# Performance work log

Measured on AMD Instinct MI355X. Metric: run time of the kernel, lower is better.

## Reference

```python
import jax, jax.numpy as jnp
import numpy as np

TAU = 1.0
PAD_IDX = 0
EOS_IDX = 3
NEG = -10000000.0

B, T, H, E, V, BN = 256, 256, 1024, 512, 32000, 512


def setup_inputs() -> dict:
    key = jax.random.key(0)
    ks = jax.random.split(key, 30)
    s = lambda *sh: 0.02
    inp = {}
    inp['input_ids'] = jax.random.randint(ks[0], (B,), 0, V)
    inp['prediction'] = jax.random.normal(ks[1], (B, V), jnp.float32)
    inp['context'] = jax.random.normal(ks[2], (B, T, 2 * H), jnp.float32)
    inp['h0'] = jax.random.normal(ks[3], (2, B, H), jnp.float32)
    inp['mask'] = jax.random.randint(ks[4], (B, 8), 0, V)
    # parameters
    inp['embedding'] = jax.random.normal(ks[5], (V, E), jnp.float32) * 0.02
    inp['ge1_w'] = jax.random.normal(ks[6], (E, E), jnp.float32) * 0.02
    inp['ge1_b'] = jnp.zeros((E,), jnp.float32)
    inp['ge2_w'] = jax.random.normal(ks[7], (E, E), jnp.float32) * 0.02
    inp['ge2_b'] = jnp.zeros((E,), jnp.float32)
    inp['att_we'] = jax.random.normal(ks[8], (2 * H, H), jnp.float32) * 0.02
    inp['att_wd'] = jax.random.normal(ks[9], (H, H), jnp.float32) * 0.02
    inp['att_v'] = jax.random.normal(ks[10], (H,), jnp.float32) * 0.02
    in0 = 2 * H + E
    inp['wih0'] = jax.random.normal(ks[11], (3 * H, in0), jnp.float32) * 0.02
    inp['whh0'] = jax.random.normal(ks[12], (3 * H, H), jnp.float32) * 0.02
    inp['bih0'] = jnp.zeros((3 * H,), jnp.float32)
    inp['bhh0'] = jnp.zeros((3 * H,), jnp.float32)
    inp['wih1'] = jax.random.normal(ks[13], (3 * H, H), jnp.float32) * 0.02
    inp['whh1'] = jax.random.normal(ks[14], (3 * H, H), jnp.float32) * 0.02
    inp['bih1'] = jnp.zeros((3 * H,), jnp.float32)
    inp['bhh1'] = jnp.zeros((3 * H,), jnp.float32)
    inp['bn0_w'] = jax.random.normal(ks[15], (3 * H + E, BN), jnp.float32) * 0.02
    inp['bn0_b'] = jnp.zeros((BN,), jnp.float32)
    inp['bn1_w'] = jax.random.normal(ks[16], (BN, V), jnp.float32) * 0.02
    inp['bn1_b'] = jnp.zeros((V,), jnp.float32)
    return inp


def _gru_cell(x, h, wih, whh, bih, bhh):
    gi = x @ wih.T + bih  # [B, 3H]
    gh = h @ whh.T + bhh
    gi_r, gi_z, gi_n = jnp.split(gi, 3, axis=1)
    gh_r, gh_z, gh_n = jnp.split(gh, 3, axis=1)
    r = jax.nn.sigmoid(gi_r + gh_r)
    z = jax.nn.sigmoid(gi_z + gh_z)
    n = jnp.tanh(gi_n + r * gh_n)
    return (1.0 - z) * n + z * h


def _forward(input_ids, prediction, context, h0, mask, embedding,
             ge1_w, ge1_b, ge2_w, ge2_b, att_we, att_wd, att_v,
             wih0, whh0, bih0, bhh0, wih1, whh1, bih1, bhh1,
             bn0_w, bn0_b, bn1_w, bn1_b):
    embs = embedding[input_ids]  # [B, E]
    # global embedding gate
    probs = jax.nn.softmax(prediction / TAU, axis=1)  # [B, V]
    emb_avg = probs @ embedding  # [B, E]
    Hg = jax.nn.sigmoid(embs @ ge1_w + ge1_b + emb_avg @ ge2_w + ge2_b)
    embs = Hg * embs + (1.0 - Hg) * emb_avg
    # bahdanau attention with query = top-layer hidden
    q = h0[-1]  # [B, H]
    scores = jnp.tanh(context @ att_we + (q @ att_wd)[:, None, :]) @ att_v  # [B, T]
    attn = jax.nn.softmax(scores, axis=1)
    c_t = jnp.einsum('bt,btd->bd', attn, context)  # [B, 2H]
    rnn_in = jnp.concatenate([embs, c_t], axis=1)  # [B, E+2H]
    h1_0 = _gru_cell(rnn_in, h0[0], wih0, whh0, bih0, bhh0)
    h1_1 = _gru_cell(h1_0, h0[1], wih1, whh1, bih1, bhh1)
    output = h1_1
    h1 = jnp.stack([h1_0, h1_1])
    b0 = jnp.tanh(jnp.concatenate([output, c_t, embs], axis=1) @ bn0_w + bn0_b)
    pred = b0 @ bn1_w + bn1_b  # [B, V]
    # masked scatter: forbid already-generated tokens, but keep PAD/EOS columns
    pad_col = pred[:, PAD_IDX]
    eos_col = pred[:, EOS_IDX]
    rows = jnp.arange(pred.shape[0])
    pred = pred.at[rows[:, None], mask].set(NEG)
    pred = pred.at[:, PAD_IDX].set(pad_col)
    pred = pred.at[:, EOS_IDX].set(eos_col)
    return pred, h1, attn


def reference(input_ids, prediction, context, h0, mask, embedding,
              ge1_w, ge1_b, ge2_w, ge2_b, att_we, att_wd, att_v,
              wih0, whh0, bih0, bhh0, wih1, whh1, bih1, bhh1,
              bn0_w, bn0_b, bn1_w, bn1_b):
    return _forward(input_ids, prediction, context, h0, mask, embedding,
                    ge1_w, ge1_b, ge2_w, ge2_b, att_we, att_wd, att_v,
                    wih0, whh0, bih0, bhh0, wih1, whh1, bih1, bhh1,
                    bn0_w, bn0_b, bn1_w, bn1_b)
```

## Files before the change

kernel.cpp:

```cpp
#include <hip/hip_runtime.h>
#include <hip/hip_bf16.h>


typedef unsigned short u16;
typedef unsigned int u32;
typedef float f32x4 __attribute__((ext_vector_type(4)));
typedef u32 u32x4 __attribute__((ext_vector_type(4)));
typedef __bf16 bf16x8 __attribute__((ext_vector_type(8)));
typedef short s16x8 __attribute__((ext_vector_type(8)));

__device__ __forceinline__ u16 f2bf(float x) {
  u32 u = __float_as_uint(x);
  u += 0x7fffu + ((u >> 16) & 1u);
  return (u16)(u >> 16);
}
__device__ __forceinline__ u32 pack2(float a, float b) {
  return (u32)f2bf(a) | ((u32)f2bf(b) << 16);
}
__device__ __forceinline__ u32 cvt2(float a, float b) {
  union { __bf16 h[2]; u32 w; } u;
  u.h[0] = (__bf16)a; u.h[1] = (__bf16)b;
  return u.w;
}
__device__ __forceinline__ float bf2f(u16 v) {
  return __uint_as_float((u32)v << 16);
}
__device__ __forceinline__ f32x4 mfma_bf16(s16x8 a, s16x8 b, f32x4 c) {
  union { s16x8 s; bf16x8 b; } ua, ub;
  ua.s = a; ub.s = b;
  return __builtin_amdgcn_mfma_f32_16x16x32_bf16(ua.b, ub.b, c, 0, 0, 0);
}
__device__ __forceinline__ void gll16(const void* g, void* l) {
  __builtin_amdgcn_global_load_lds((__attribute__((address_space(1))) void*)g,
                                   (__attribute__((address_space(3))) void*)l,
                                   16, 0, 0);
}
__device__ __forceinline__ float sigf(float x) { return 1.0f / (1.0f + __expf(-x)); }

__global__ __launch_bounds__(256) void k_cvt8(const float* __restrict__ s,
                                              u16* __restrict__ d)
{
  size_t i = ((size_t)blockIdx.x * 256 + threadIdx.x) * 8;
  const size_t stride = (size_t)gridDim.x * 2048;
  for (; i < 134217728ull; i += stride) {
    float4 a = *(const float4*)(s + i);
    float4 b = *(const float4*)(s + i + 4);
    u32x4 w = {cvt2(a.x, a.y), cvt2(a.z, a.w), cvt2(b.x, b.y), cvt2(b.z, b.w)};
    *(u32x4*)(d + i) = w;
  }
}

__global__ __launch_bounds__(256, 2) void k_scores_bf(
    const u16* __restrict__ A, const u16* __restrict__ weT,
    const float* __restrict__ qd, const float* __restrict__ att_v,
    float* __restrict__ scores)
{
  __shared__ u16 As[3][4096];
  __shared__ u16 Bs[3][8192];

  const int tid = threadIdx.x;
  const int lane = tid & 63, wid = tid >> 6;
  const int l15 = lane & 15, lg = lane >> 4;
  const int wm = wid >> 1, wn = wid & 1;

  const int f = blockIdx.x;
  const int xcd = f & 7, slot = f >> 3;
  const int ntile = slot & 3;
  const int mtile = (slot >> 2) * 8 + xcd;
  const int n0 = ntile * 256;
  const int m0 = mtile * 128;
  const int b = mtile >> 1;

  const int sslot = ((lane & 3) ^ ((lane >> 3) & 3)) * 8;
  size_t asrc[2];
#pragma unroll
  for (int i = 0; i < 2; ++i)
    asrc[i] = (size_t)(m0 + wid * 32 + i * 16 + (lane >> 2)) * 2048 + sslot;
  size_t bsrc[4];
#pragma unroll
  for (int i = 0; i < 4; ++i)
    bsrc[i] = (size_t)(n0 + wid * 64 + i * 16 + (lane >> 2)) * 2048 + sslot;

  const int rslot = (lg ^ ((l15 >> 1) & 3)) * 8;
  int aoff[4], boff[8];
#pragma unroll
  for (int mf = 0; mf < 4; ++mf) aoff[mf] = (wm * 64 + mf * 16 + l15) * 32 + rslot;
#pragma unroll
  for (int nf = 0; nf < 8; ++nf) boff[nf] = (wn * 128 + nf * 16 + l15) * 32 + rslot;

  f32x4 acc[4][8];
#pragma unroll
  for (int mf = 0; mf < 4; ++mf)
#pragma unroll
    for (int nf = 0; nf < 8; ++nf) acc[mf][nf] = (f32x4){0.f, 0.f, 0.f, 0.f};

  u16* As0 = &As[0][0];
  u16* Bs0 = &Bs[0][0];

#pragma unroll
  for (int t = 0; t < 2; ++t) {
#pragma unroll
    for (int i = 0; i < 2; ++i)
      gll16(A + asrc[i] + (size_t)t * 32, As0 + t * 4096 + wid * 1024 + i * 512);
#pragma unroll
    for (int i = 0; i < 4; ++i)
      gll16(weT + bsrc[i] + (size_t)t * 32, Bs0 + t * 8192 + wid * 2048 + i * 512);
  }

  int cur = 0, stg = 2;
  for (int kt = 0; kt < 64; ++kt) {
    if (kt < 63) asm volatile("s_waitcnt vmcnt(6)" ::: "memory");
    else         asm volatile("s_waitcnt vmcnt(0)" ::: "memory");
    __builtin_amdgcn_s_barrier();
    __builtin_amdgcn_sched_barrier(0);
    if (kt + 2 < 64) {
#pragma unroll
      for (int i = 0; i < 2; ++i)
        gll16(A + asrc[i] + (size_t)(kt + 2) * 32,
              As0 + stg * 4096 + wid * 1024 + i * 512);
#pragma unroll
      for (int i = 0; i < 4; ++i)
        gll16(weT + bsrc[i] + (size_t)(kt + 2) * 32,
              Bs0 + stg * 8192 + wid * 2048 + i * 512);
    }
    s16x8 af[4], bf[8];
#pragma unroll
    for (int mf = 0; mf < 4; ++mf)
      af[mf] = *(const s16x8*)(As0 + cur * 4096 + aoff[mf]);
#pragma unroll
    for (int nf = 0; nf < 8; ++nf)
      bf[nf] = *(const s16x8*)(Bs0 + cur * 8192 + boff[nf]);
    __builtin_amdgcn_s_setprio(1);
#pragma unroll
    for (int nf = 0; nf < 8; ++nf)
#pragma unroll
      for (int mf = 0; mf < 4; ++mf)
        acc[mf][nf] = mfma_bf16(af[mf], bf[nf], acc[mf][nf]);
    __builtin_amdgcn_s_setprio(0);
    cur = (cur == 2) ? 0 : cur + 1;
    stg = (stg == 2) ? 0 : stg + 1;
  }

  float rp[4][4] = {{0.f, 0.f, 0.f, 0.f}, {0.f, 0.f, 0.f, 0.f},
                    {0.f, 0.f, 0.f, 0.f}, {0.f, 0.f, 0.f, 0.f}};
#pragma unroll
  for (int nf = 0; nf < 8; ++nf) {
    int col = n0 + wn * 128 + nf * 16 + l15;
    float qv = qd[(size_t)b * 1024 + col];
    float vv = att_v[col];
#pragma unroll
    for (int mf = 0; mf < 4; ++mf)
#pragma unroll
      for (int e = 0; e < 4; ++e)
        rp[mf][e] += tanhf(acc[mf][nf][e] + qv) * vv;
  }
#pragma unroll
  for (int d = 1; d < 16; d <<= 1)
#pragma unroll
    for (int mf = 0; mf < 4; ++mf)
#pragma unroll
      for (int e = 0; e < 4; ++e)
        rp[mf][e] += __shfl_xor(rp[mf][e], d);
  if (l15 == 0) {
#pragma unroll
    for (int mf = 0; mf < 4; ++mf)
#pragma unroll
      for (int e = 0; e < 4; ++e)
        atomicAdd(&scores[(size_t)m0 + wm * 64 + mf * 16 + lg * 4 + e], rp[mf][e]);
  }
}

__global__ __launch_bounds__(256, 3) void k_scores(
    const float* __restrict__ ctx, const u16* __restrict__ weT,
    const float* __restrict__ qd, const float* __restrict__ att_v,
    float* __restrict__ scores)
{
  __shared__ u16 As[2][4096];
  __shared__ u16 Bs[2][4096];

  const int tid = threadIdx.x;
  const int lane = tid & 63, wid = tid >> 6;
  const int l15 = lane & 15, lg = lane >> 4;
  const int wm = wid >> 1, wn = wid & 1;
  const int n0 = blockIdx.x * 128;
  const int m0 = blockIdx.y * 128;
  const int b = blockIdx.y >> 1;

  const int r0 = tid >> 3, c4 = tid & 7;
  const float* actx = ctx + (size_t)(m0 + r0) * 2048 + c4 * 4;
  const int awoff = r0 * 32 + c4 * 4;

  size_t bsrc[2];
#pragma unroll
  for (int i = 0; i < 2; ++i)
    bsrc[i] = (size_t)(n0 + (wid * 2 + i) * 16 + (lane >> 2)) * 2048 + (size_t)(lane & 3) * 8;

  int aoff[4], boff[4];
#pragma unroll
  for (int mf = 0; mf < 4; ++mf) aoff[mf] = (wm * 64 + mf * 16 + l15) * 32 + lg * 8;
#pragma unroll
  for (int nf = 0; nf < 4; ++nf) boff[nf] = (wn * 64 + nf * 16 + l15) * 32 + lg * 8;

  f32x4 acc[4][4];
#pragma unroll
  for (int mf = 0; mf < 4; ++mf)
#pragma unroll
    for (int nf = 0; nf < 4; ++nf) acc[mf][nf] = (f32x4){0.f, 0.f, 0.f, 0.f};

  {
#pragma unroll
    for (int i = 0; i < 2; ++i)
      gll16(weT + bsrc[i], &Bs[0][(wid * 2 + i) * 512]);
#pragma unroll
    for (int j = 0; j < 4; ++j) {
      float4 av = *(const float4*)(actx + (size_t)(j * 32) * 2048);
      u32* w = (u32*)&As[0][awoff + j * 1024];
      w[0] = cvt2(av.x, av.y); w[1] = cvt2(av.z, av.w);
    }
  }
  __syncthreads();

  for (int kt = 0; kt < 64; ++kt) {
    const int cur = kt & 1, nxt = cur ^ 1;
    const bool pf = (kt < 63);
    float4 av[4];
    if (pf) {
#pragma unroll
      for (int i = 0; i < 2; ++i)
        gll16(weT + bsrc[i] + (size_t)(kt + 1) * 32, &Bs[nxt][(wid * 2 + i) * 512]);
#pragma unroll
      for (int j = 0; j < 4; ++j)
        av[j] = *(const float4*)(actx + (size_t)(j * 32) * 2048 + (kt + 1) * 32);
    }
    s16x8 af[4], bf[4];
#pragma unroll
    for (int mf = 0; mf < 4; ++mf) af[mf] = *(const s16x8*)(&As[cur][0] + aoff[mf]);
#pragma unroll
    for (int nf = 0; nf < 4; ++nf) bf[nf] = *(const s16x8*)(&Bs[cur][0] + boff[nf]);
#pragma unroll
    for (int nf = 0; nf < 4; ++nf)
#pragma unroll
      for (int mf = 0; mf < 4; ++mf)
        acc[mf][nf] = mfma_bf16(af[mf], bf[nf], acc[mf][nf]);
    if (pf) {
#pragma unroll
      for (int j = 0; j < 4; ++j) {
        u32* w = (u32*)&As[nxt][awoff + j * 1024];
        w[0] = cvt2(av[j].x, av[j].y); w[1] = cvt2(av[j].z, av[j].w);
      }
    }
    __syncthreads();
  }

  float rp[4][4] = {{0.f, 0.f, 0.f, 0.f}, {0.f, 0.f, 0.f, 0.f},
                    {0.f, 0.f, 0.f, 0.f}, {0.f, 0.f, 0.f, 0.f}};
#pragma unroll
  for (int nf = 0; nf < 4; ++nf) {
    int col = n0 + wn * 64 + nf * 16 + l15;
    float qv = qd[(size_t)b * 1024 + col];
    float vv = att_v[col];
#pragma unroll
    for (int mf = 0; mf < 4; ++mf)
#pragma unroll
      for (int e = 0; e < 4; ++e)
        rp[mf][e] += tanhf(acc[mf][nf][e] + qv) * vv;
  }
#pragma unroll
  for (int d = 1; d < 16; d <<= 1)
#pragma unroll
    for (int mf = 0; mf < 4; ++mf)
#pragma unroll
      for (int e = 0; e < 4; ++e)
        rp[mf][e] += __shfl_xor(rp[mf][e], d);
  if (l15 == 0) {
#pragma unroll
    for (int mf = 0; mf < 4; ++mf)
#pragma unroll
      for (int e = 0; e < 4; ++e)
        atomicAdd(&scores[(size_t)m0 + wm * 64 + mf * 16 + lg * 4 + e], rp[mf][e]);
  }
}

template <int MODE>
__global__ __launch_bounds__(256, 2) void k_gemm(
    const u16* __restrict__ A, const float* __restrict__ W,
    float* __restrict__ C, const float* __restrict__ bias,
    int N, int K, int ksteps_per, int tot_ksteps, int atomic_mode)
{
  __shared__ u16 As[2][8192];
  __shared__ u16 Bs[2][2048];
  const int tid = threadIdx.x, lane = tid & 63, wid = tid >> 6;
  const int l15 = lane & 15, lg = lane >> 4;
  const int m0 = blockIdx.x * 256;
  const int n0 = blockIdx.y * 64;
  const int kc0 = blockIdx.z * ksteps_per;
  int kcn = tot_ksteps - kc0;
  if (kcn > ksteps_per) kcn = ksteps_per;

  size_t asrc[4];
#pragma unroll
  for (int j = 0; j < 4; ++j)
    asrc[j] = (size_t)(m0 + wid * 64 + j * 16 + (lane >> 2)) * K + (size_t)(lane & 3) * 8;
  int aoff[4], boff[4];
#pragma unroll
  for (int mf = 0; mf < 4; ++mf) aoff[mf] = (wid * 64 + mf * 16 + l15) * 32 + lg * 8;
#pragma unroll
  for (int nf = 0; nf < 4; ++nf) boff[nf] = (nf * 16 + l15) * 32 + lg * 8;

  const int b_row = tid >> 2, b_c8 = tid & 3;
  const int b_kk = tid >> 3, b_c4 = tid & 7;

  f32x4 acc[4][4];
#pragma unroll
  for (int mf = 0; mf < 4; ++mf)
#pragma unroll
    for (int nf = 0; nf < 4; ++nf) acc[mf][nf] = (f32x4){0.f, 0.f, 0.f, 0.f};

  {
#pragma unroll
    for (int j = 0; j < 4; ++j)
      gll16(A + asrc[j] + (size_t)kc0 * 32, &As[0][wid * 2048 + j * 512]);
    if (MODE == 0) {
      const float* p = W + (size_t)(n0 + b_row) * K + (size_t)kc0 * 32 + b_c8 * 8;
      float4 v0 = *(const float4*)p, v1 = *(const float4*)(p + 4);
      u32* w = (u32*)&Bs[0][b_row * 32 + b_c8 * 8];
      w[0] = pack2(v0.x, v0.y); w[1] = pack2(v0.z, v0.w);
      w[2] = pack2(v1.x, v1.y); w[3] = pack2(v1.z, v1.w);
    } else {
      const float* p = W + (size_t)(kc0 * 32 + b_kk) * N + n0 + b_c4 * 4;
      float4 v0 = *(const float4*)p;
      float4 v1 = *(const float4*)(p + 32);
      int r0 = b_c4 * 4, r1 = 32 + b_c4 * 4;
      Bs[0][(r0 + 0) * 32 + b_kk] = f2bf(v0.x);
      Bs[0][(r0 + 1) * 32 + b_kk] = f2bf(v0.y);
      Bs[0][(r0 + 2) * 32 + b_kk] = f2bf(v0.z);
      Bs[0][(r0 + 3) * 32 + b_kk] = f2bf(v0.w);
      Bs[0][(r1 + 0) * 32 + b_kk] = f2bf(v1.x);
      Bs[0][(r1 + 1) * 32 + b_kk] = f2bf(v1.y);
      Bs[0][(r1 + 2) * 32 + b_kk] = f2bf(v1.z);
      Bs[0][(r1 + 3) * 32 + b_kk] = f2bf(v1.w);
    }
  }
  __syncthreads();

  for (int s = 0; s < kcn; ++s) {
    const int cur = s & 1, nxt = cur ^ 1;
    const bool pf = (s + 1 < kcn);
    const int ktn = kc0 + s + 1;
    float4 v0, v1;
    if (pf) {
#pragma unroll
      for (int j = 0; j < 4; ++j)
        gll16(A + asrc[j] + (size_t)ktn * 32, &As[nxt][wid * 2048 + j * 512]);
      if (MODE == 0) {
        const float* p = W + (size_t)(n0 + b_row) * K + (size_t)ktn * 32 + b_c8 * 8;
        v0 = *(const float4*)p; v1 = *(const float4*)(p + 4);
      } else {
        const float* p = W + (size_t)(ktn * 32 + b_kk) * N + n0 + b_c4 * 4;
        v0 = *(const float4*)p;
        v1 = *(const float4*)(p + 32);
      }
    }
    s16x8 af[4], bf[4];
#pragma unroll
    for (int mf = 0; mf < 4; ++mf) af[mf] = *(const s16x8*)(&As[cur][0] + aoff[mf]);
#pragma unroll
    for (int nf = 0; nf < 4; ++nf) bf[nf] = *(const s16x8*)(&Bs[cur][0] + boff[nf]);
#pragma unroll
    for (int nf = 0; nf < 4; ++nf)
#pragma unroll
      for (int mf = 0; mf < 4; ++mf)
        acc[mf][nf] = mfma_bf16(af[mf], bf[nf], acc[mf][nf]);
    if (pf) {
      if (MODE == 0) {
        u32* w = (u32*)&Bs[nxt][b_row * 32 + b_c8 * 8];
        w[0] = pack2(v0.x, v0.y); w[1] = pack2(v0.z, v0.w);
        w[2] = pack2(v1.x, v1.y); w[3] = pack2(v1.z, v1.w);
      } else {
        int r0 = b_c4 * 4, r1 = 32 + b_c4 * 4;
        Bs[nxt][(r0 + 0) * 32 + b_kk] = f2bf(v0.x);
        Bs[nxt][(r0 + 1) * 32 + b_kk] = f2bf(v0.y);
        Bs[nxt][(r0 + 2) * 32 + b_kk] = f2bf(v0.z);
        Bs[nxt][(r0 + 3) * 32 + b_kk] = f2bf(v0.w);
        Bs[nxt][(r1 + 0) * 32 + b_kk] = f2bf(v1.x);
        Bs[nxt][(r1 + 1) * 32 + b_kk] = f2bf(v1.y);
        Bs[nxt][(r1 + 2) * 32 + b_kk] = f2bf(v1.z);
        Bs[nxt][(r1 + 3) * 32 + b_kk] = f2bf(v1.w);
      }
    }
    __syncthreads();
  }

  const size_t Ns = (size_t)N;
#pragma unroll
  for (int mf = 0; mf < 4; ++mf)
#pragma unroll
    for (int nf = 0; nf < 4; ++nf) {
      int col = n0 + nf * 16 + l15;
#pragma unroll
      for (int e = 0; e < 4; ++e) {
        int row = m0 + wid * 64 + mf * 16 + lg * 4 + e;
        float v = acc[mf][nf][e];
        if (atomic_mode) atomicAdd(&C[row * Ns + col], v);
        else C[row * Ns + col] = v + (bias ? bias[col] : 0.0f);
      }
    }
}

__global__ __launch_bounds__(256) void k_prep(
    const float* __restrict__ we, u16* __restrict__ weT,
    const float* __restrict__ h0, u16* __restrict__ h0_bf,
    const int* __restrict__ ids, const float* __restrict__ emb,
    float* __restrict__ e0, u16* __restrict__ e0b)
{
  __shared__ float t[32][33];
  const int bid = blockIdx.x, tid = threadIdx.x;
  if (bid < 2048) {
    const int n0 = (bid & 31) * 32, k0 = (bid >> 5) * 32;
#pragma unroll
    for (int p = 0; p < 4; ++p) {
      int e = tid + p * 256, r = e >> 5, c = e & 31;
      t[r][c] = we[(size_t)(k0 + r) * 1024 + n0 + c];
    }
    __syncthreads();
#pragma unroll
    for (int p = 0; p < 4; ++p) {
      int e = tid + p * 256, n = e >> 5, k = e & 31;
      weT[(size_t)(n0 + n) * 2048 + k0 + k] = f2bf(t[k][n]);
    }
  } else if (bid < 4096) {
    int i = (bid - 2048) * 256 + tid;
    h0_bf[i] = f2bf(h0[i]);
  } else {
    int b = bid - 4096;
    int id = ids[b];
    for (int i = tid; i < 512; i += 256) {
      float v = emb[(size_t)id * 512 + i];
      e0[(size_t)b * 512 + i] = v;
      e0b[(size_t)b * 512 + i] = f2bf(v);
    }
  }
}

__global__ void k_cast(const float* __restrict__ s, u16* __restrict__ d, int n)
{
  int i = blockIdx.x * 256 + threadIdx.x;
  if (i < n) d[i] = f2bf(s[i]);
}

__global__ __launch_bounds__(1024) void k_softmax_pred(const float* __restrict__ pred,
                                                       u16* __restrict__ probs)
{
  __shared__ u16 xrow[32000];
  __shared__ float smM[16], smS[16];
  const int row = blockIdx.x, tid = threadIdx.x;
  const float* x = pred + (size_t)row * 32000;
  float m = -3.0e38f, s = 0.f;
  for (int i = tid; i < 32000; i += 1024) {
    u16 bv = f2bf(x[i]);
    xrow[i] = bv;
    float vr = bf2f(bv);
    if (vr > m) { s = s * __expf(m - vr) + 1.0f; m = vr; }
    else s += __expf(vr - m);
  }
#pragma unroll
  for (int d = 1; d < 64; d <<= 1) {
    float mo = __shfl_xor(m, d), so = __shfl_xor(s, d);
    float M = fmaxf(m, mo);
    s = s * __expf(m - M) + so * __expf(mo - M);
    m = M;
  }
  if ((tid & 63) == 0) { smM[tid >> 6] = m; smS[tid >> 6] = s; }
  __syncthreads();
  float M = -3.0e38f;
#pragma unroll
  for (int w = 0; w < 16; ++w) M = fmaxf(M, smM[w]);
  float S = 0.f;
#pragma unroll
  for (int w = 0; w < 16; ++w) S += smS[w] * __expf(smM[w] - M);
  float inv = 1.0f / S;
  for (int i = tid; i < 32000; i += 1024)
    probs[(size_t)row * 32000 + i] = f2bf(__expf(bf2f(xrow[i]) - M) * inv);
}

__global__ __launch_bounds__(256) void k_softmax_sc(const float* __restrict__ sc,
                                                    float* __restrict__ attn)
{
  __shared__ float sm[4];
  const int row = blockIdx.x, tid = threadIdx.x;
  float x = sc[(size_t)row * 256 + tid];
  float mx = x;
#pragma unroll
  for (int d = 1; d < 64; d <<= 1) mx = fmaxf(mx, __shfl_xor(mx, d));
  if ((tid & 63) == 0) sm[tid >> 6] = mx;
  __syncthreads();
  mx = fmaxf(fmaxf(sm[0], sm[1]), fmaxf(sm[2], sm[3]));
  float e = __expf(x - mx);
  float s = e;
#pragma unroll
  for (int d = 1; d < 64; d <<= 1) s += __shfl_xor(s, d);
  __syncthreads();
  if ((tid & 63) == 0) sm[tid >> 6] = s;
  __syncthreads();
  s = sm[0] + sm[1] + sm[2] + sm[3];
  attn[(size_t)row * 256 + tid] = e / s;
}

__global__ __launch_bounds__(256) void k_attn_ct(
    const float* __restrict__ sc, const u16* __restrict__ ctxb,
    float* __restrict__ attn, float* __restrict__ c_t)
{
  __shared__ float sm[4];
  __shared__ float att[256];
  const int b = blockIdx.y, tid = threadIdx.x;
  float x = sc[(size_t)b * 256 + tid];
  float mx = x;
#pragma unroll
  for (int d = 1; d < 64; d <<= 1) mx = fmaxf(mx, __shfl_xor(mx, d));
  if ((tid & 63) == 0) sm[tid >> 6] = mx;
  __syncthreads();
  mx = fmaxf(fmaxf(sm[0], sm[1]), fmaxf(sm[2], sm[3]));
  float e = __expf(x - mx);
  float s = e;
#pragma unroll
  for (int d = 1; d < 64; d <<= 1) s += __shfl_xor(s, d);
  __syncthreads();
  if ((tid & 63) == 0) sm[tid >> 6] = s;
  __syncthreads();
  s = sm[0] + sm[1] + sm[2] + sm[3];
  float a = e / s;
  att[tid] = a;
  if (blockIdx.x == 0) attn[(size_t)b * 256 + tid] = a;
  __syncthreads();

  const int d0 = blockIdx.x * 512 + tid * 2;
  const u16* cp = ctxb + (size_t)b * 524288 + d0;
  float a0 = 0.f, a1 = 0.f;
#pragma unroll 8
  for (int t = 0; t < 256; ++t) {
    float av = att[t];
    ushort2 v = *(const ushort2*)(cp + (size_t)t * 2048);
    a0 += av * bf2f(v.x); a1 += av * bf2f(v.y);
  }
  float2* o = (float2*)(c_t + (size_t)b * 2048 + d0);
  *o = (float2){a0, a1};
}

__global__ __launch_bounds__(256) void k_ct(const float* __restrict__ ctx,
                                            const float* __restrict__ attn,
                                            float* __restrict__ c_t)
{
  const int b = blockIdx.y;
  const int d0 = blockIdx.x * 512 + threadIdx.x * 2;
  const float2* cp = (const float2*)(ctx + (size_t)b * 524288 + d0);
  const float* ar = attn + (size_t)b * 256;
  float ax = 0.f, ay = 0.f;
#pragma unroll 4
  for (int t = 0; t < 256; ++t) {
    float a = ar[t];
    float2 v = cp[(size_t)t * 1024];
    ax += a * v.x; ay += a * v.y;
  }
  c_t[(size_t)b * 2048 + d0] = ax;
  c_t[(size_t)b * 2048 + d0 + 1] = ay;
}

__global__ void k_gate_cat(const float* __restrict__ gepre, const float* __restrict__ b1,
                           const float* __restrict__ b2, const float* __restrict__ e0,
                           const float* __restrict__ ea, float* __restrict__ embs,
                           const float* __restrict__ ct, u16* __restrict__ out)
{
  int i = blockIdx.x * 256 + threadIdx.x;
  int m = i / 2560, c = i - m * 2560;
  float v;
  if (c < 512) {
    int idx = m * 512 + c;
    float hg = sigf(gepre[idx] + b1[c] + b2[c]);
    v = hg * e0[idx] + (1.0f - hg) * ea[idx];
    embs[idx] = v;
  } else {
    v = ct[(size_t)m * 2048 + (c - 512)];
  }
  out[i] = f2bf(v);
}

__global__ void k_gru(const float* __restrict__ gi, const float* __restrict__ gh,
                      const float* __restrict__ bih, const float* __restrict__ bhh,
                      const float* __restrict__ hprev, float* __restrict__ hout,
                      u16* __restrict__ hout_bf)
{
  int i = blockIdx.x * 256 + threadIdx.x;
  int m = i >> 10, h = i & 1023;
  const float* gim = gi + (size_t)m * 3072;
  const float* ghm = gh + (size_t)m * 3072;
  float r = sigf(gim[h] + bih[h] + ghm[h] + bhh[h]);
  float z = sigf(gim[1024 + h] + bih[1024 + h] + ghm[1024 + h] + bhh[1024 + h]);
  float n = tanhf(gim[2048 + h] + bih[2048 + h] + r * (ghm[2048 + h] + bhh[2048 + h]));
  float hv = (1.0f - z) * n + z * hprev[i];
  hout[i] = hv;
  if (hout_bf) hout_bf[i] = f2bf(hv);
}

__global__ void k_cat_bn0(const float* __restrict__ h11, const float* __restrict__ ct,
                          const float* __restrict__ embs, u16* __restrict__ out)
{
  int i = blockIdx.x * 256 + threadIdx.x;
  int m = i / 3584, c = i - m * 3584;
  float v;
  if (c < 1024) v = h11[(size_t)m * 1024 + c];
  else if (c < 3072) v = ct[(size_t)m * 2048 + (c - 1024)];
  else v = embs[(size_t)m * 512 + (c - 3072)];
  out[i] = f2bf(v);
}

__global__ void k_bn0(const float* __restrict__ pre, const float* __restrict__ bias,
                      u16* __restrict__ b0b)
{
  int i = blockIdx.x * 256 + threadIdx.x;
  int nn = i & 511;
  b0b[i] = f2bf(tanhf(pre[i] + bias[nn]));
}

__global__ void k_mask(const int* __restrict__ mask, float* __restrict__ pred)
{
  int t = blockIdx.x * 256 + threadIdx.x;
  if (t >= 2048) return;
  int b = t >> 3;
  int col = mask[t];
  if (col != 0 && col != 3) pred[(size_t)b * 32000 + col] = -10000000.0f;
}

extern "C" void kernel_launch(void* const* d_in, const int* in_sizes, int n_in,
                              void* d_out, int out_size, void* d_ws, size_t ws_size,
                              hipStream_t stream)
{
  const int*   input_ids = (const int*)d_in[0];
  const float* prediction= (const float*)d_in[1];
  const float* context   = (const float*)d_in[2];
  const float* h0        = (const float*)d_in[3];
  const int*   maskp     = (const int*)d_in[4];
  const float* embedding = (const float*)d_in[5];
  const float* ge1_w = (const float*)d_in[6];
  const float* ge1_b = (const float*)d_in[7];
  const float* ge2_w = (const float*)d_in[8];
  const float* ge2_b = (const float*)d_in[9];
  const float* att_we = (const float*)d_in[10];
  const float* att_wd = (const float*)d_in[11];
  const float* att_v  = (const float*)d_in[12];
  const float* wih0 = (const float*)d_in[13];
  const float* whh0 = (const float*)d_in[14];
  const float* bih0 = (const float*)d_in[15];
  const float* bhh0 = (const float*)d_in[16];
  const float* wih1 = (const float*)d_in[17];
  const float* whh1 = (const float*)d_in[18];
  const float* bih1 = (const float*)d_in[19];
  const float* bhh1 = (const float*)d_in[20];
  const float* bn0_w = (const float*)d_in[21];
  const float* bn0_b = (const float*)d_in[22];
  const float* bn1_w = (const float*)d_in[23];
  const float* bn1_b = (const float*)d_in[24];

  float* out = (float*)d_out;
  float* out_pred = out;
  float* out_h1_0 = out + 8192000;
  float* out_h1_1 = out + 8454144;
  float* out_attn = out + 8716288;

  char* ws = (char*)d_ws;
  float* qd      = (float*)(ws + 0);
  float* emb_avg = (float*)(ws + 1048576);
  float* gepre   = (float*)(ws + 1572864);
  float* gi0     = (float*)(ws + 2097152);
  float* gh0     = (float*)(ws + 5242880);
  float* gi1     = (float*)(ws + 8388608);
  float* gh1     = (float*)(ws + 11534336);
  float* bn0pre  = (float*)(ws + 14680064);
  float* scores  = (float*)(ws + 15204352);
  const size_t MS_BYTES = 15466496;
  float* c_t     = (float*)(ws + 15466496);
  float* embs0   = (float*)(ws + 17563648);
  float* embs    = (float*)(ws + 18087936);
  u16* weT       = (u16*)(ws + 18612224);
  u16* h0_bf     = (u16*)(ws + 22806528);
  u16* embs0_bf  = (u16*)(ws + 23855104);
  u16* probs_bf  = (u16*)(ws + 24117248);
  u16* embavg_bf = (u16*)(ws + 40501248);
  u16* rnnin_bf  = (u16*)(ws + 40763392);
  u16* h1_0_bf   = (u16*)(ws + 42074112);
  u16* bn0in_bf  = (u16*)(ws + 42598400);
  u16* b0_bf     = (u16*)(ws + 44433408);
  u16* ctx_bf    = (u16*)(ws + 44695552);
  const bool big = ws_size >= 44695552ull + 268435456ull;

  (void)in_sizes; (void)n_in; (void)out_size;

  hipMemsetAsync(ws, 0, MS_BYTES, stream);

  if (big) k_cvt8<<<8192, 256, 0, stream>>>(context, ctx_bf);
  k_prep<<<4352, 256, 0, stream>>>(att_we, weT, h0, h0_bf, input_ids, embedding,
                                   embs0, embs0_bf);
  k_softmax_pred<<<256, 1024, 0, stream>>>(prediction, probs_bf);

  k_gemm<1><<<dim3(1, 16, 8), 256, 0, stream>>>(h0_bf + 262144, att_wd, qd, nullptr,
                                                1024, 1024, 4, 32, 1);
  if (big)
    k_scores_bf<<<2048, 256, 0, stream>>>(ctx_bf, weT, qd, att_v, scores);
  else
    k_scores<<<dim3(8, 512), 256, 0, stream>>>(context, weT, qd, att_v, scores);

  k_gemm<1><<<dim3(1, 8, 50), 256, 0, stream>>>(probs_bf, embedding, emb_avg, nullptr,
                                                512, 32000, 20, 1000, 1);
  k_cast<<<512, 256, 0, stream>>>(emb_avg, embavg_bf, 131072);
  k_gemm<1><<<dim3(1, 8, 4), 256, 0, stream>>>(embs0_bf, ge1_w, gepre, nullptr,
                                               512, 512, 4, 16, 1);
  k_gemm<1><<<dim3(1, 8, 4), 256, 0, stream>>>(embavg_bf, ge2_w, gepre, nullptr,
                                               512, 512, 4, 16, 1);

  if (big) {
    k_attn_ct<<<dim3(4, 256), 256, 0, stream>>>(scores, ctx_bf, out_attn, c_t);
  } else {
    k_softmax_sc<<<256, 256, 0, stream>>>(scores, out_attn);
    k_ct<<<dim3(4, 256), 256, 0, stream>>>(context, out_attn, c_t);
  }

  k_gate_cat<<<2560, 256, 0, stream>>>(gepre, ge1_b, ge2_b, embs0, emb_avg,
                                       embs, c_t, rnnin_bf);

  k_gemm<0><<<dim3(1, 48, 5), 256, 0, stream>>>(rnnin_bf, wih0, gi0, nullptr,
                                                3072, 2560, 16, 80, 1);
  k_gemm<0><<<dim3(1, 48, 4), 256, 0, stream>>>(h0_bf, whh0, gh0, nullptr,
                                                3072, 1024, 8, 32, 1);
  k_gru<<<1024, 256, 0, stream>>>(gi0, gh0, bih0, bhh0, h0, out_h1_0, h1_0_bf);
  k_gemm<0><<<dim3(1, 48, 4), 256, 0, stream>>>(h1_0_bf, wih1, gi1, nullptr,
                                                3072, 1024, 8, 32, 1);
  k_gemm<0><<<dim3(1, 48, 4), 256, 0, stream>>>(h0_bf + 262144, whh1, gh1, nullptr,
                                                3072, 1024, 8, 32, 1);
  k_gru<<<1024, 256, 0, stream>>>(gi1, gh1, bih1, bhh1, h0 + 262144, out_h1_1, nullptr);

  k_cat_bn0<<<3584, 256, 0, stream>>>(out_h1_1, c_t, embs, bn0in_bf);
  k_gemm<1><<<dim3(1, 8, 16), 256, 0, stream>>>(bn0in_bf, bn0_w, bn0pre, nullptr,
                                                512, 3584, 7, 112, 1);
  k_bn0<<<512, 256, 0, stream>>>(bn0pre, bn0_b, b0_bf);
  k_gemm<1><<<dim3(1, 500, 1), 256, 0, stream>>>(b0_bf, bn1_w, out_pred, bn1_b,
                                                 32000, 512, 16, 16, 0);
  k_mask<<<8, 256, 0, stream>>>(maskp, out_pred);
}
```

Before: 836.0 us.

## Enlarge scores GEMM tile to 256x256 with eight waves and double buffering

Result: slower. 3.194 ms (+282.1%).

```diff
diff --git a/kernel.cpp b/kernel.cpp
--- a/kernel.cpp
+++ b/kernel.cpp
@@ -50,13 +50,13 @@
   }
 }
 
-__global__ __launch_bounds__(256, 2) void k_scores_bf(
+__global__ __launch_bounds__(512, 4) void k_scores_bf(
     const u16* __restrict__ A, const u16* __restrict__ weT,
     const float* __restrict__ qd, const float* __restrict__ att_v,
     float* __restrict__ scores)
 {
-  __shared__ u16 As[3][4096];
-  __shared__ u16 Bs[3][8192];
+  __shared__ u16 As[2][8192];
+  __shared__ u16 Bs[2][8192];
 
   const int tid = threadIdx.x;
   const int lane = tid & 63, wid = tid >> 6;
@@ -68,18 +68,16 @@
   const int ntile = slot & 3;
   const int mtile = (slot >> 2) * 8 + xcd;
   const int n0 = ntile * 256;
-  const int m0 = mtile * 128;
-  const int b = mtile >> 1;
+  const int m0 = mtile * 256;
+  const int b = mtile;
 
   const int sslot = ((lane & 3) ^ ((lane >> 3) & 3)) * 8;
-  size_t asrc[2];
-#pragma unroll
-  for (int i = 0; i < 2; ++i)
-    asrc[i] = (size_t)(m0 + wid * 32 + i * 16 + (lane >> 2)) * 2048 + sslot;
-  size_t bsrc[4];
-#pragma unroll
-  for (int i = 0; i < 4; ++i)
-    bsrc[i] = (size_t)(n0 + wid * 64 + i * 16 + (lane >> 2)) * 2048 + sslot;
+  size_t asrc[2], bsrc[2];
+#pragma unroll
+  for (int i = 0; i < 2; ++i) {
+    asrc[i] = (size_t)(m0 + (wid * 2 + i) * 16 + (lane >> 2)) * 2048 + sslot;
+    bsrc[i] = (size_t)(n0 + (wid * 2 + i) * 16 + (lane >> 2)) * 2048 + sslot;
+  }
 
   const int rslot = (lg ^ ((l15 >> 1) & 3)) * 8;
   int aoff[4], boff[8];
@@ -94,42 +92,29 @@
 #pragma unroll
     for (int nf = 0; nf < 8; ++nf) acc[mf][nf] = (f32x4){0.f, 0.f, 0.f, 0.f};
 
-  u16* As0 = &As[0][0];
-  u16* Bs0 = &Bs[0][0];
-
 #pragma unroll
   for (int t = 0; t < 2; ++t) {
 #pragma unroll
     for (int i = 0; i < 2; ++i)
-      gll16(A + asrc[i] + (size_t)t * 32, As0 + t * 4096 + wid * 1024 + i * 512);
-#pragma unroll
-    for (int i = 0; i < 4; ++i)
-      gll16(weT + bsrc[i] + (size_t)t * 32, Bs0 + t * 8192 + wid * 2048 + i * 512);
-  }
-
-  int cur = 0, stg = 2;
+      gll16(A + asrc[i] + (size_t)t * 32, &As[t][(wid * 2 + i) * 512]);
+#pragma unroll
+    for (int i = 0; i < 2; ++i)
+      gll16(weT + bsrc[i] + (size_t)t * 32, &Bs[t][(wid * 2 + i) * 512]);
+  }
+
   for (int kt = 0; kt < 64; ++kt) {
-    if (kt < 63) asm volatile("s_waitcnt vmcnt(6)" ::: "memory");
+    const int cur = kt & 1;
+    if (kt < 63) asm volatile("s_waitcnt vmcnt(4)" ::: "memory");
     else         asm volatile("s_waitcnt vmcnt(0)" ::: "memory");
     __builtin_amdgcn_s_barrier();
     __builtin_amdgcn_sched_barrier(0);
-    if (kt + 2 < 64) {
-#pragma unroll
-      for (int i = 0; i < 2; ++i)
-        gll16(A + asrc[i] + (size_t)(kt + 2) * 32,
-              As0 + stg * 4096 + wid * 1024 + i * 512);
-#pragma unroll
-      for (int i = 0; i < 4; ++i)
-        gll16(weT + bsrc[i] + (size_t)(kt + 2) * 32,
-              Bs0 + stg * 8192 + wid * 2048 + i * 512);
-    }
     s16x8 af[4], bf[8];
 #pragma unroll
     for (int mf = 0; mf < 4; ++mf)
-      af[mf] = *(const s16x8*)(As0 + cur * 4096 + aoff[mf]);
+      af[mf] = *(const s16x8*)(&As[cur][0] + aoff[mf]);
 #pragma unroll
     for (int nf = 0; nf < 8; ++nf)
-      bf[nf] = *(const s16x8*)(Bs0 + cur * 8192 + boff[nf]);
+      bf[nf] = *(const s16x8*)(&Bs[cur][0] + boff[nf]);
     __builtin_amdgcn_s_setprio(1);
 #pragma unroll
     for (int nf = 0; nf < 8; ++nf)
@@ -137,8 +122,16 @@
       for (int mf = 0; mf < 4; ++mf)
         acc[mf][nf] = mfma_bf16(af[mf], bf[nf], acc[mf][nf]);
     __builtin_amdgcn_s_setprio(0);
-    cur = (cur == 2) ? 0 : cur + 1;
-    stg = (stg == 2) ? 0 : stg + 1;
+    __builtin_amdgcn_s_barrier();
+    __builtin_amdgcn_sched_barrier(0);
+    if (kt + 2 < 64) {
+#pragma unroll
+      for (int i = 0; i < 2; ++i)
+        gll16(A + asrc[i] + (size_t)(kt + 2) * 32, &As[cur][(wid * 2 + i) * 512]);
+#pragma unroll
+      for (int i = 0; i < 2; ++i)
+        gll16(weT + bsrc[i] + (size_t)(kt + 2) * 32, &Bs[cur][(wid * 2 + i) * 512]);
+    }
   }
 
   float rp[4][4] = {{0.f, 0.f, 0.f, 0.f}, {0.f, 0.f, 0.f, 0.f},
@@ -704,7 +697,7 @@
   k_gemm<1><<<dim3(1, 16, 8), 256, 0, stream>>>(h0_bf + 262144, att_wd, qd, nullptr,
                                                 1024, 1024, 4, 32, 1);
   if (big)
-    k_scores_bf<<<2048, 256, 0, stream>>>(ctx_bf, weT, qd, att_v, scores);
+    k_scores_bf<<<1024, 512, 0, stream>>>(ctx_bf, weT, qd, att_v, scores);
   else
     k_scores<<<dim3(8, 512), 256, 0, stream>>>(context, weT, qd, att_v, scores);
 
```
